# Kernel tuning notes

Hardware: AMD Instinct MI355X
Metric: run time of the kernel (lower is better)

## Reference

```python
import jax, jax.numpy as jnp
import numpy as np

N_NODES = 131072
N_EDGES = 2097152
B = 256
NODES_PER_GRAPH = 512  # uniform graphs -> to_dense_batch == reshape
F_IN = 74
D = 128
L = 3
EPS = 1e-5


def setup_inputs() -> dict:
    key = jax.random.key(0)
    ks = jax.random.split(key, 12)
    x = jax.random.normal(ks[0], (N_NODES, F_IN), dtype=jnp.float32)
    edge_index = jax.random.randint(ks[1], (2, N_EDGES), 0, N_NODES, dtype=jnp.int32)
    batch = (jnp.arange(N_NODES, dtype=jnp.int32) // NODES_PER_GRAPH)
    s = 1.0 / np.sqrt(D)
    W_init = jax.random.uniform(ks[2], (F_IN, D), jnp.float32, -s, s)
    W_gcn = jax.random.uniform(ks[3], (L, D, D), jnp.float32, -s, s)
    b_gcn = jnp.zeros((L, D), jnp.float32)
    gamma = jnp.ones((L, D), jnp.float32)
    beta = jnp.zeros((L, D), jnp.float32)
    W_res = jax.random.uniform(ks[4], (L, D, D), jnp.float32, -s, s)
    b_res = jax.random.uniform(ks[5], (L, D), jnp.float32, -s, s)
    return {"x": x, "edge_index": edge_index, "batch": batch, "W_init": W_init,
            "W_gcn": W_gcn, "b_gcn": b_gcn, "gamma": gamma, "beta": beta,
            "W_res": W_res, "b_res": b_res}


def _gcn_conv(x, src, tgt, norm, W, b):
    # PyG GCNConv: h = x @ W ; out[tgt] += norm * h[src] ; + bias
    h = x @ W                                    # [N, D]
    msg = h[src] * norm[:, None]                 # [E+N, D] gather (memory-bound)
    out = jax.ops.segment_sum(msg, tgt, num_segments=N_NODES)
    return out + b


def _batchnorm(x, g, bta):
    mean = jnp.mean(x, axis=0)
    var = jnp.var(x, axis=0)  # biased, matches torch BN training forward
    return (x - mean) * jax.lax.rsqrt(var + EPS) * g + bta


def reference(x, edge_index, batch, W_init, W_gcn, b_gcn, gamma, beta, W_res, b_res):
    # add self loops once; symmetric deg^{-1/2} normalization (PyG default)
    loops = jnp.arange(N_NODES, dtype=edge_index.dtype)
    src = jnp.concatenate([edge_index[0], loops])
    tgt = jnp.concatenate([edge_index[1], loops])
    deg = jax.ops.segment_sum(jnp.ones_like(src, dtype=jnp.float32), tgt,
                              num_segments=N_NODES)
    dinv = jnp.where(deg > 0, jax.lax.rsqrt(jnp.maximum(deg, 1.0)), 0.0)
    norm = dinv[src] * dinv[tgt]

    h = x @ W_init                               # init_transform (no bias)
    for i in range(L):
        conv = _gcn_conv(h, src, tgt, norm, W_gcn[i], b_gcn[i])
        h_new = jax.nn.relu(_batchnorm(conv, gamma[i], beta[i]))
        h = h_new + (h @ W_res[i] + b_res[i])
    # to_dense_batch with uniform NODES_PER_GRAPH -> reshape, all mask=True
    return h.reshape(B, NODES_PER_GRAPH, D)
```

## Files before the change

### kernel.cpp

```cpp
#include <hip/hip_runtime.h>

#define NN 131072
#define NE 2097152
#define DD 128
#define LL 3

#define NB 256
#define BSH 9
#define TILE (NE / NB)

typedef __attribute__((ext_vector_type(8))) short short8;
typedef __attribute__((ext_vector_type(4))) float f32x4;

__device__ __forceinline__ ushort f2bf(float f) {
    uint u = __float_as_uint(f);
    return (ushort)((u + 0x7fffu + ((u >> 16) & 1u)) >> 16);
}
__device__ __forceinline__ float bflo(uint u) { return __uint_as_float(u << 16); }
__device__ __forceinline__ float bfhi(uint u) { return __uint_as_float(u & 0xffff0000u); }

__global__ __launch_bounds__(256) void k_zero(float* __restrict__ bns) {
    int i = blockIdx.x * 256 + threadIdx.x;
    if (i < 768) bns[i] = 0.0f;
}

__global__ __launch_bounds__(256) void kA_count(const int* __restrict__ tgt,
                                                int* __restrict__ blockHist) {
    __shared__ int hist[NB];
    const int t = threadIdx.x, blk = blockIdx.x;
    hist[t] = 0;
    __syncthreads();
    const int base = blk * TILE;
#pragma unroll 8
    for (int j = 0; j < TILE / 256; ++j)
        atomicAdd(&hist[tgt[base + j * 256 + t] >> BSH], 1);
    __syncthreads();
    blockHist[t * NB + blk] = hist[t];
}

__global__ __launch_bounds__(256) void kA_scan(int* __restrict__ blockHist,
                                               int* __restrict__ bstart) {
    __shared__ int part[NB];
    const int t = threadIdx.x;
    int4* bh = (int4*)(blockHist + t * NB);
    int run = 0;
    int4 tmp[NB / 4];
#pragma unroll 8
    for (int j = 0; j < NB / 4; ++j) tmp[j] = bh[j];
#pragma unroll 8
    for (int j = 0; j < NB / 4; ++j) {
        int4 v = tmp[j];
        int a = run; run += v.x;
        int b = run; run += v.y;
        int c = run; run += v.z;
        int d = run; run += v.w;
        tmp[j] = make_int4(a, b, c, d);
    }
    part[t] = run;
    __syncthreads();
    for (int off = 1; off < NB; off <<= 1) {
        int v = part[t];
        int u = (t >= off) ? part[t - off] : 0;
        __syncthreads();
        part[t] = v + u;
        __syncthreads();
    }
    const int excl = part[t] - run;
    bstart[t] = excl;
    if (t == NB - 1) bstart[NB] = part[t];
#pragma unroll 8
    for (int j = 0; j < NB / 4; ++j) {
        int4 v = tmp[j];
        bh[j] = make_int4(v.x + excl, v.y + excl, v.z + excl, v.w + excl);
    }
}

__global__ __launch_bounds__(256) void kA_scatter(const int* __restrict__ src,
                                                  const int* __restrict__ tgt,
                                                  const int* __restrict__ chunkBase,
                                                  uint* __restrict__ packed) {
    __shared__ int cur[NB];
    const int t = threadIdx.x, blk = blockIdx.x;
    cur[t] = chunkBase[t * NB + blk];
    __syncthreads();
    const int base = blk * TILE;
#pragma unroll 4
    for (int j = 0; j < TILE / 256; ++j) {
        const int e = base + j * 256 + t;
        const int tg = tgt[e], s = src[e];
        const int b = tg >> BSH;
        const int pos = atomicAdd(&cur[b], 1);
        packed[pos] = (uint)s | ((uint)(tg & ((1 << BSH) - 1)) << 17);
    }
}

__global__ __launch_bounds__(256) void kB_sort(const uint* __restrict__ packed,
                                               const int* __restrict__ bstart,
                                               int* __restrict__ rowp,
                                               float* __restrict__ dinv,
                                               int* __restrict__ ssrc) {
    __shared__ int cnt[1 << BSH];
    __shared__ int pscan[256];
    const int t = threadIdx.x, b = blockIdx.x;
    const int e0 = bstart[b], e1 = bstart[b + 1];
    cnt[t] = 0; cnt[t + 256] = 0;
    __syncthreads();
    for (int e = e0 + t; e < e1; e += 256)
        atomicAdd(&cnt[packed[e] >> 17], 1);
    __syncthreads();
    const int c0 = cnt[2 * t], c1 = cnt[2 * t + 1];
    pscan[t] = c0 + c1;
    __syncthreads();
    for (int off = 1; off < 256; off <<= 1) {
        int v = pscan[t];
        int u = (t >= off) ? pscan[t - off] : 0;
        __syncthreads();
        pscan[t] = v + u;
        __syncthreads();
    }
    const int ex0 = pscan[t] - c0 - c1;
    const int ex1 = ex0 + c0;
    const int n0 = (b << BSH) + 2 * t;
    rowp[n0] = e0 + ex0;
    rowp[n0 + 1] = e0 + ex1;
    dinv[n0] = rsqrtf((float)(c0 + 1));
    dinv[n0 + 1] = rsqrtf((float)(c1 + 1));
    if (b == NB - 1 && t == 255) rowp[NN] = e1;
    __syncthreads();
    cnt[2 * t] = ex0;
    cnt[2 * t + 1] = ex1;
    __syncthreads();
    for (int e = e0 + t; e < e1; e += 256) {
        const uint p = packed[e];
        const int pos = atomicAdd(&cnt[p >> 17], 1);
        ssrc[e0 + pos] = (int)(p & 0x1FFFFu);
    }
}

__global__ __launch_bounds__(256) void k_prepw(const float* __restrict__ Wi,
                                               const float* __restrict__ Wg,
                                               const float* __restrict__ Wr,
                                               ushort* __restrict__ wt) {
    const int id = blockIdx.x * 256 + threadIdx.x;
    const int m = id >> 14;
    const int c = (id >> 7) & 127;
    const int k = id & 127;
    float v;
    if (m == 0)      v = (k < 74) ? Wi[k * DD + c] : 0.0f;
    else if (m <= 3) v = Wg[(size_t)(m - 1) * DD * DD + k * DD + c];
    else             v = Wr[(size_t)(m - 4) * DD * DD + k * DD + c];
    wt[id] = f2bf(v);
}

__global__ __launch_bounds__(256) void k_convx(const float* __restrict__ x,
                                               uint* __restrict__ xb) {
    const size_t id = (size_t)blockIdx.x * 256 + threadIdx.x;
    const int n = (int)(id >> 6);
    const int k0 = (int)(id & 63) * 2;
    float v0 = (k0 < 74) ? x[(size_t)n * 74 + k0] : 0.0f;
    float v1 = (k0 + 1 < 74) ? x[(size_t)n * 74 + k0 + 1] : 0.0f;
    xb[id] = (uint)f2bf(v0) | ((uint)f2bf(v1) << 16);
}

template <int MODE>
__global__ __launch_bounds__(256) void k_mgemm(const ushort* A,
                                               const ushort* __restrict__ Bt,
                                               ushort* outb,
                                               float* __restrict__ outf,
                                               const float* __restrict__ conv,
                                               const float* __restrict__ ss,
                                               const float* __restrict__ bres,
                                               float* __restrict__ bnsums) {
    __shared__ ushort As[16384];
    __shared__ ushort Bs[16384];
    __shared__ float sred[256];
    const int t = threadIdx.x;
    const int w = t >> 6, l = t & 63;
    const int lc = l & 15, lr = l >> 4;
    const size_t row0 = (size_t)blockIdx.x * 128;

    for (int ch = w * 8; ch < w * 8 + 8; ++ch) {
        const int row = ch * 4 + lr;
        const int kb = (lc * 16) ^ ((row & 7) << 4);
        const ushort* srcA = A + (row0 + row) * DD + (kb >> 1);
        const ushort* srcB = Bt + (size_t)row * DD + (kb >> 1);
        __builtin_amdgcn_global_load_lds(
            (const __attribute__((address_space(1))) void*)srcA,
            (__attribute__((address_space(3))) void*)(As + ch * 512), 16, 0, 0);
        __builtin_amdgcn_global_load_lds(
            (const __attribute__((address_space(1))) void*)srcB,
            (__attribute__((address_space(3))) void*)(Bs + ch * 512), 16, 0, 0);
    }
    if (MODE == 1) sred[t] = 0.0f;
    __syncthreads();

    f32x4 acc[2][8] = {};
    const char* Ab = (const char*)As;
    const char* Bb = (const char*)Bs;
#pragma unroll
    for (int kk = 0; kk < 4; ++kk) {
        const int kb = kk * 64 + lr * 16;
        short8 a[2];
#pragma unroll
        for (int m = 0; m < 2; ++m) {
            const int r = w * 32 + m * 16 + lc;
            a[m] = *(const short8*)(Ab + r * 256 + (kb ^ ((r & 7) << 4)));
        }
#pragma unroll
        for (int n = 0; n < 8; ++n) {
            const int c = n * 16 + lc;
            short8 b = *(const short8*)(Bb + c * 256 + (kb ^ ((c & 7) << 4)));
            acc[0][n] = __builtin_amdgcn_mfma_f32_16x16x32_bf16(a[0], b, acc[0][n], 0, 0, 0);
            acc[1][n] = __builtin_amdgcn_mfma_f32_16x16x32_bf16(a[1], b, acc[1][n], 0, 0, 0);
        }
    }

    if (MODE == 0) {
#pragma unroll
        for (int m = 0; m < 2; ++m)
#pragma unroll
            for (int n = 0; n < 8; ++n) {
                const int c = n * 16 + lc;
#pragma unroll
                for (int j = 0; j < 4; ++j) {
                    const size_t r = row0 + w * 32 + m * 16 + lr * 4 + j;
                    outb[r * DD + c] = f2bf(acc[m][n][j]);
                }
            }
    } else if (MODE == 1) {
#pragma unroll
        for (int n = 0; n < 8; ++n) {
            const int c = n * 16 + lc;
            float ps = 0.0f, ps2 = 0.0f;
#pragma unroll
            for (int m = 0; m < 2; ++m)
#pragma unroll
                for (int j = 0; j < 4; ++j) {
                    const size_t r = row0 + w * 32 + m * 16 + lr * 4 + j;
                    const float v = acc[m][n][j];
                    outf[r * DD + c] = v;
                    ps += v; ps2 += v * v;
                }
            atomicAdd(&sred[c], ps);
            atomicAdd(&sred[DD + c], ps2);
        }
        __syncthreads();
        atomicAdd(&bnsums[t], sred[t]);
    } else {
        float scv[8], shv[8], bbv[8];
#pragma unroll
        for (int n = 0; n < 8; ++n) {
            const int c = n * 16 + lc;
            scv[n] = ss[c]; shv[n] = ss[DD + c]; bbv[n] = bres[c];
        }
#pragma unroll
        for (int m = 0; m < 2; ++m)
#pragma unroll
            for (int n = 0; n < 8; ++n) {
                const int c = n * 16 + lc;
#pragma unroll
                for (int j = 0; j < 4; ++j) {
                    const size_t r = row0 + w * 32 + m * 16 + lr * 4 + j;
                    const float cv = conv[r * DD + c];
                    const float v = fmaxf(cv * scv[n] + shv[n], 0.0f) + acc[m][n][j] + bbv[n];
                    outb[r * DD + c] = f2bf(v);
                    if (MODE == 3) outf[r * DD + c] = v;
                }
            }
    }
}

__global__ __launch_bounds__(256) void k_aggregate(const int* __restrict__ row,
                                                   const int* __restrict__ ssrc,
                                                   const float* __restrict__ dinv,
                                                   const uint* __restrict__ hb,
                                                   uint* __restrict__ aggb) {
    const int n = blockIdx.x * 4 + (threadIdx.x >> 6);
    const int l = threadIdx.x & 63;
    const float dn = dinv[n];
    const uint u = hb[((uint)n << 6) + l];
    const float dn2 = dn * dn;
    float2 acc = make_float2(bflo(u) * dn2, bfhi(u) * dn2);
    const int e0 = row[n], e1 = row[n + 1];
    for (int base = e0; base < e1; base += 64) {
        const int cnt = min(64, e1 - base);
        int sv = 0; float dv = 0.0f;
        if (l < cnt) { sv = ssrc[base + l]; dv = dinv[sv] * dn; }
        for (int i = 0; i < cnt; i += 8) {
            uint vv[8]; float nm[8];
#pragma unroll
            for (int j = 0; j < 8; ++j) {
                const int s = __shfl(sv, i + j);
                nm[j] = __shfl(dv, i + j);
                vv[j] = hb[((uint)s << 6) + l];
            }
#pragma unroll
            for (int j = 0; j < 8; ++j) {
                acc.x += nm[j] * bflo(vv[j]);
                acc.y += nm[j] * bfhi(vv[j]);
            }
        }
    }
    aggb[((uint)n << 6) + l] = (uint)f2bf(acc.x) | ((uint)f2bf(acc.y) << 16);
}

__global__ void k_bnfin(const float* __restrict__ sums,
                        const float* __restrict__ gamma,
                        const float* __restrict__ beta,
                        float* __restrict__ ss) {
    int c = threadIdx.x;
    const float invN = 1.0f / (float)NN;
    float mean = sums[c] * invN;
    float var = sums[DD + c] * invN - mean * mean;
    float sc = gamma[c] * rsqrtf(var + 1e-5f);
    ss[c] = sc;
    ss[DD + c] = beta[c] - mean * sc;
}

extern "C" void kernel_launch(void* const* d_in, const int* in_sizes, int n_in,
                              void* d_out, int out_size, void* d_ws, size_t ws_size,
                              hipStream_t stream) {
    const float* x      = (const float*)d_in[0];
    const int*   ei     = (const int*)d_in[1];
    const float* W_init = (const float*)d_in[3];
    const float* W_gcn  = (const float*)d_in[4];
    const float* gamma  = (const float*)d_in[6];
    const float* beta   = (const float*)d_in[7];
    const float* W_res  = (const float*)d_in[8];
    const float* b_res  = (const float*)d_in[9];

    float* h = (float*)d_out;
    char* p = (char*)d_ws;
    ushort* aggb = (ushort*)p;           p += (size_t)NN * DD * 2;
    ushort* hb  = (ushort*)p;            p += (size_t)NN * DD * 2;
    float*  conv = (float*)p;            p += (size_t)NN * DD * 4;
    uint*   xb   = (uint*)conv;
    float*  dinv = (float*)p;            p += (size_t)NN * 4;
    float*  bns  = (float*)p;            p += 768 * 4;
    float*  ss   = (float*)p;            p += 256 * 4;
    ushort* wt   = (ushort*)p;           p += 7 * 16384 * 2;
    int* blockHist = (int*)p;            p += (size_t)NB * NB * 4;
    int* bstart  = (int*)p;              p += (NB + 1) * 4 + 4;
    uint* packed = (uint*)p;             p += (size_t)NE * 4;
    int* rowp    = (int*)p;              p += ((size_t)NN + 1) * 4 + 4;
    int* ssrc    = (int*)p;

    const int* srcp = ei;
    const int* tgtp = ei + NE;

    k_zero<<<3, 256, 0, stream>>>(bns);
    kA_count<<<NB, 256, 0, stream>>>(tgtp, blockHist);
    kA_scan<<<1, 256, 0, stream>>>(blockHist, bstart);
    kA_scatter<<<NB, 256, 0, stream>>>(srcp, tgtp, blockHist, packed);
    kB_sort<<<NB, 256, 0, stream>>>(packed, bstart, rowp, dinv, ssrc);

    k_prepw<<<7 * 16384 / 256, 256, 0, stream>>>(W_init, W_gcn, W_res, wt);
    k_convx<<<NN * 64 / 256, 256, 0, stream>>>(x, xb);

    k_mgemm<0><<<NN / 128, 256, 0, stream>>>((const ushort*)xb, wt, hb,
                                             nullptr, nullptr, nullptr, nullptr, nullptr);

    for (int i = 0; i < LL; ++i) {
        k_aggregate<<<NN / 4, 256, 0, stream>>>(rowp, ssrc, dinv,
                                                (const uint*)hb, (uint*)aggb);
        k_mgemm<1><<<NN / 128, 256, 0, stream>>>(aggb, wt + (size_t)(1 + i) * 16384,
                                                 nullptr, conv, nullptr, nullptr,
                                                 nullptr, bns + i * 256);
        k_bnfin<<<1, 128, 0, stream>>>(bns + i * 256, gamma + i * DD,
                                       beta + i * DD, ss);
        if (i < LL - 1)
            k_mgemm<2><<<NN / 128, 256, 0, stream>>>(hb, wt + (size_t)(4 + i) * 16384,
                                                     hb, nullptr, conv, ss,
                                                     b_res + i * DD, nullptr);
        else
            k_mgemm<3><<<NN / 128, 256, 0, stream>>>(hb, wt + (size_t)(4 + i) * 16384,
                                                     hb, h, conv, ss,
                                                     b_res + i * DD, nullptr);
    }
}
```

Measured before the change: 579.4 us.

## Store conv output in bf16 and vectorize edge aggregation with 16-byte row loads

The GCN conv intermediate is written and read back as bf16 instead of fp32, halving its global traffic between the GEMM passes. The aggregation kernel now has each 16-lane group gather a full 256-byte feature row with uint4 loads and process four edges in parallel per wavefront, then reduce across groups with shuffles. This aims to cut memory-instruction count and improve gather efficiency, at the cost of extra rounding on the conv values and more registers per lane.

```diff
diff --git a/kernel.cpp b/kernel.cpp
--- a/kernel.cpp
+++ b/kernel.cpp
@@ -167,7 +167,7 @@
                                                const ushort* __restrict__ Bt,
                                                ushort* outb,
                                                float* __restrict__ outf,
-                                               const float* __restrict__ conv,
+                                               const ushort* __restrict__ convb,
                                                const float* __restrict__ ss,
                                                const float* __restrict__ bres,
                                                float* __restrict__ bnsums) {
@@ -238,7 +238,7 @@
                 for (int j = 0; j < 4; ++j) {
                     const size_t r = row0 + w * 32 + m * 16 + lr * 4 + j;
                     const float v = acc[m][n][j];
-                    outf[r * DD + c] = v;
+                    outb[r * DD + c] = f2bf(v);
                     ps += v; ps2 += v * v;
                 }
             atomicAdd(&sred[c], ps);
@@ -261,7 +261,7 @@
 #pragma unroll
                 for (int j = 0; j < 4; ++j) {
                     const size_t r = row0 + w * 32 + m * 16 + lr * 4 + j;
-                    const float cv = conv[r * DD + c];
+                    const float cv = __uint_as_float((uint)convb[r * DD + c] << 16);
                     const float v = fmaxf(cv * scv[n] + shv[n], 0.0f) + acc[m][n][j] + bbv[n];
                     outb[r * DD + c] = f2bf(v);
                     if (MODE == 3) outf[r * DD + c] = v;
@@ -277,31 +277,57 @@
                                                    uint* __restrict__ aggb) {
     const int n = blockIdx.x * 4 + (threadIdx.x >> 6);
     const int l = threadIdx.x & 63;
+    const int g = l >> 4;
+    const int sub = l & 15;
     const float dn = dinv[n];
-    const uint u = hb[((uint)n << 6) + l];
-    const float dn2 = dn * dn;
-    float2 acc = make_float2(bflo(u) * dn2, bfhi(u) * dn2);
+
+    float acc[8];
+    {
+        const uint4 v = *(const uint4*)(hb + ((size_t)n << 6) + sub * 4);
+        const float dn2 = (g == 0) ? dn * dn : 0.0f;
+        acc[0] = dn2 * bflo(v.x); acc[1] = dn2 * bfhi(v.x);
+        acc[2] = dn2 * bflo(v.y); acc[3] = dn2 * bfhi(v.y);
+        acc[4] = dn2 * bflo(v.z); acc[5] = dn2 * bfhi(v.z);
+        acc[6] = dn2 * bflo(v.w); acc[7] = dn2 * bfhi(v.w);
+    }
+
     const int e0 = row[n], e1 = row[n + 1];
     for (int base = e0; base < e1; base += 64) {
         const int cnt = min(64, e1 - base);
         int sv = 0; float dv = 0.0f;
         if (l < cnt) { sv = ssrc[base + l]; dv = dinv[sv] * dn; }
-        for (int i = 0; i < cnt; i += 8) {
-            uint vv[8]; float nm[8];
-#pragma unroll
-            for (int j = 0; j < 8; ++j) {
-                const int s = __shfl(sv, i + j);
-                nm[j] = __shfl(dv, i + j);
-                vv[j] = hb[((uint)s << 6) + l];
+        for (int i = 0; i < cnt; i += 16) {
+            uint4 vv[4]; float nm[4];
+#pragma unroll
+            for (int j = 0; j < 4; ++j) {
+                const int e = i + j * 4 + g;
+                const int s = __shfl(sv, e);
+                nm[j] = __shfl(dv, e);
+                vv[j] = *(const uint4*)(hb + ((size_t)s << 6) + sub * 4);
             }
 #pragma unroll
-            for (int j = 0; j < 8; ++j) {
-                acc.x += nm[j] * bflo(vv[j]);
-                acc.y += nm[j] * bfhi(vv[j]);
+            for (int j = 0; j < 4; ++j) {
+                acc[0] += nm[j] * bflo(vv[j].x); acc[1] += nm[j] * bfhi(vv[j].x);
+                acc[2] += nm[j] * bflo(vv[j].y); acc[3] += nm[j] * bfhi(vv[j].y);
+                acc[4] += nm[j] * bflo(vv[j].z); acc[5] += nm[j] * bfhi(vv[j].z);
+                acc[6] += nm[j] * bflo(vv[j].w); acc[7] += nm[j] * bfhi(vv[j].w);
             }
         }
     }
-    aggb[((uint)n << 6) + l] = (uint)f2bf(acc.x) | ((uint)f2bf(acc.y) << 16);
+
+#pragma unroll
+    for (int k = 0; k < 8; ++k) {
+        acc[k] += __shfl_xor(acc[k], 16);
+        acc[k] += __shfl_xor(acc[k], 32);
+    }
+    if (g == 0) {
+        uint4 o;
+        o.x = (uint)f2bf(acc[0]) | ((uint)f2bf(acc[1]) << 16);
+        o.y = (uint)f2bf(acc[2]) | ((uint)f2bf(acc[3]) << 16);
+        o.z = (uint)f2bf(acc[4]) | ((uint)f2bf(acc[5]) << 16);
+        o.w = (uint)f2bf(acc[6]) | ((uint)f2bf(acc[7]) << 16);
+        *(uint4*)(aggb + ((size_t)n << 6) + sub * 4) = o;
+    }
 }
 
 __global__ void k_bnfin(const float* __restrict__ sums,
@@ -332,9 +358,9 @@
     float* h = (float*)d_out;
     char* p = (char*)d_ws;
     ushort* aggb = (ushort*)p;           p += (size_t)NN * DD * 2;
-    ushort* hb  = (ushort*)p;            p += (size_t)NN * DD * 2;
-    float*  conv = (float*)p;            p += (size_t)NN * DD * 4;
-    uint*   xb   = (uint*)conv;
+    ushort* hb   = (ushort*)p;           p += (size_t)NN * DD * 2;
+    ushort* convb = (ushort*)p;          p += (size_t)NN * DD * 2;
+    uint*   xb   = (uint*)convb;
     float*  dinv = (float*)p;            p += (size_t)NN * 4;
     float*  bns  = (float*)p;            p += 768 * 4;
     float*  ss   = (float*)p;            p += 256 * 4;
@@ -364,17 +390,17 @@
         k_aggregate<<<NN / 4, 256, 0, stream>>>(rowp, ssrc, dinv,
                                                 (const uint*)hb, (uint*)aggb);
         k_mgemm<1><<<NN / 128, 256, 0, stream>>>(aggb, wt + (size_t)(1 + i) * 16384,
-                                                 nullptr, conv, nullptr, nullptr,
+                                                 convb, nullptr, nullptr, nullptr,
                                                  nullptr, bns + i * 256);
         k_bnfin<<<1, 128, 0, stream>>>(bns + i * 256, gamma + i * DD,
                                        beta + i * DD, ss);
         if (i < LL - 1)
             k_mgemm<2><<<NN / 128, 256, 0, stream>>>(hb, wt + (size_t)(4 + i) * 16384,
-                                                     hb, nullptr, conv, ss,
+                                                     hb, nullptr, convb, ss,
                                                      b_res + i * DD, nullptr);
         else
             k_mgemm<3><<<NN / 128, 256, 0, stream>>>(hb, wt + (size_t)(4 + i) * 16384,
-                                                     hb, h, conv, ss,
+                                                     hb, h, convb, ss,
                                                      b_res + i * DD, nullptr);
     }
 }
```

Result: slower. 607.6 us (+4.9%).
